# Performance work log

Measured on AMD Instinct MI355X. Metric: run time of the kernel, lower is better.

## Reference

```python
import jax, jax.numpy as jnp
import numpy as np

PS = 2      # patch_size
TOPK = 3    # topk


def setup_inputs() -> dict:
    key = jax.random.key(0)
    x = jax.random.normal(key, (8, 128, 64, 64), dtype=jnp.float32)
    alpha = jnp.asarray(5.0, dtype=jnp.float32)  # nn.Parameter alpha
    return {"x": x, "alpha": alpha}


def _forward(x, alpha):
    ps = PS
    b, c, h, w = x.shape
    nph, npw = h // ps, w // ps
    npatch = nph * npw
    pa = ps * ps
    # F.normalize(p=2, dim=-3) with torch eps=1e-12
    norm = jnp.maximum(jnp.sqrt(jnp.sum(x * x, axis=1, keepdims=True)), 1e-12)
    x = x / norm
    # patchify -> [b, c, npatch, patch_area] (patches h-major, pixels row-major)
    xp = x.reshape(b, c, nph, ps, npw, ps).transpose(0, 1, 2, 4, 3, 5)
    xp = xp.reshape(b, c, npatch, pa)
    diag_idx = jnp.arange(ps) * (ps + 1)  # [0, 3] for ps=2
    # gather diagonal pixels of each patch -> [b, ps, npatch, c]
    xd = xp[:, :, :, diag_idx].transpose(0, 3, 2, 1)
    # patch correlation matmul -> [b, ps, npatch, npatch]
    corr = jnp.einsum('bpnc,bpmc->bpnm', xd, xd)
    avg = jnp.mean(corr, axis=1, keepdims=True)
    s = jnp.concatenate([corr, avg], axis=1)  # [b, ps+1, npatch, npatch]
    # ZeroWindow gaussian mask (rat_s=0.05); channel index = patch center (r,c)
    sr, sc = 0.05 * nph, 0.05 * npw
    rr = jnp.arange(nph, dtype=jnp.float32)
    cc = jnp.arange(npw, dtype=jnp.float32)
    cent_r, cent_c = jnp.meshgrid(rr, cc, indexing='ij')
    cent_r = cent_r.reshape(npatch)
    cent_c = cent_c.reshape(npatch)
    gr = jnp.exp(-(rr[None, :] - cent_r[:, None]) ** 2 / (2.0 * sr * sr))  # [npatch, nph]
    gc = jnp.exp(-(cc[None, :] - cent_c[:, None]) ** 2 / (2.0 * sc * sc))  # [npatch, npw]
    mask = (1.0 - gr[:, :, None] * gc[:, None, :]).reshape(npatch, npatch)
    s = s * mask[None, None]
    a = s * alpha
    # double (row + col) softmax
    s = jax.nn.softmax(a, axis=-1) * jax.nn.softmax(a, axis=-2)
    # expand avg channel to all patch pixels, scatter diagonal channels back
    new_x = jnp.broadcast_to(s[:, -1:], (b, pa, npatch, npatch))
    new_x = new_x.at[:, diag_idx].set(s[:, :ps])
    # un-patchify second npatch axis to spatial [b, npatch, h, w]
    y = jnp.swapaxes(new_x, 1, 3)  # [b, npatch, npatch, pa]
    y = y.reshape(b, npatch, nph, npw, ps, ps).transpose(0, 1, 2, 4, 3, 5)
    y = y.reshape(b, npatch, h, w)
    # topk over the npatch axis (dim=-3)
    vals = jax.lax.top_k(jnp.moveaxis(y, 1, -1), TOPK)[0]  # [b, h, w, k]
    return jnp.moveaxis(vals, -1, 1)  # [b, k, h, w]


def reference(x, alpha):
    return _forward(x, alpha)
```

## Files before the change

### kernel.cpp

```cpp
#include <hip/hip_runtime.h>
#include <hip/hip_bf16.h>
#include <math.h>

#define NB 8
#define NC 128
#define NH 64
#define NW 64
#define NP 1024
#define TWO_SIG2 5.12f
#define LOG2E 1.44269504089f

static const size_t PSUM_OFF_B = 0;
static const size_t PBUF_OFF_B = (size_t)NB * 3 * 4 * NP * 4;
static const size_t XD_OFF_B   = PBUF_OFF_B + (size_t)NB * NP * 3 * 4 * 3 * 4;

typedef __bf16 bf16x8 __attribute__((ext_vector_type(8)));
typedef float f32x4 __attribute__((ext_vector_type(4)));

#define INSERT3(v, A, Bq, Cq)                          \
  {                                                    \
    const float _na = fmaxf(A, (v));                   \
    const float _nb = __builtin_amdgcn_fmed3f(A, Bq, (v)); \
    Cq = __builtin_amdgcn_fmed3f(Bq, Cq, (v));         \
    A = _na;                                           \
    Bq = _nb;                                          \
  }

#define MERGE3(a0, a1, a2, b0, b1, b2)       \
  {                                          \
    const float _x1 = fmaxf(a0, b0);         \
    const float _y1 = fminf(a0, b0);         \
    const float _x2 = fmaxf(a1, b1);         \
    const float _z  = fmaxf(a2, b2);         \
    a0 = _x1;                                \
    a1 = fmaxf(_y1, _x2);                    \
    a2 = fmaxf(fminf(_y1, _x2), _z);         \
  }

__global__ __launch_bounds__(1024) void k1_norm(const float* __restrict__ x,
                                                __hip_bfloat16* __restrict__ xd) {
  __shared__ __align__(16) float tile[NC * 65];
  const int chunk = blockIdx.x;
  const int p = blockIdx.y;
  const int b = blockIdx.z;
  const int t = threadIdx.x;
  const int pix = t & 63;
  const int cw = t >> 6;
  const int nbase = chunk * 64;

  {
    const int n = nbase + pix;
    const int i = ((n >> 5) << 1) + p;
    const int jf = (n & 31);
    const float* xb = x + (size_t)b * NC * NH * NW + (size_t)i * NW;
    for (int cc = 0; cc < 8; ++cc) {
      const int c = (cc << 4) + cw;
      const float2 v2 = ((const float2*)(xb + (size_t)c * NH * NW))[jf];
      tile[c * 65 + pix] = (p == 0) ? v2.x : v2.y;
    }
  }
  __syncthreads();

  const int lane = t & 63;
  const int w = t >> 6;
  for (int pg = 0; pg < 4; ++pg) {
    const int pixel = (pg << 4) + w;
    const float v0 = tile[lane * 65 + pixel];
    const float v1 = tile[(lane + 64) * 65 + pixel];
    float ss = v0 * v0 + v1 * v1;
#pragma unroll
    for (int m = 32; m >= 1; m >>= 1) ss += __shfl_xor(ss, m, 64);
    const float inv = 1.0f / fmaxf(sqrtf(ss), 1e-12f);
    __hip_bfloat16* xr = xd + ((size_t)((b * 2 + p) * NP) + nbase + pixel) * NC;
    xr[lane] = __float2bfloat16(v0 * inv);
    xr[lane + 64] = __float2bfloat16(v1 * inv);
  }
}

__global__ __launch_bounds__(256) void k2_sums(const ushort* __restrict__ xd,
                                               const float* __restrict__ alpha_p,
                                               float* __restrict__ psum) {
  __shared__ __align__(16) __bf16 Bs[2][64 * 136];
  const int t = threadIdx.x;
  const float K = (*alpha_p) * LOG2E;
  const float Cm = -(LOG2E / TWO_SIG2);

  const int cchunk = blockIdx.x;
  const int rowtile = blockIdx.y;
  const int b = blockIdx.z;
  const int i0 = rowtile << 6;
  const int jb = cchunk << 8;

  const int wave = t >> 6;
  const int lane = t & 63;
  const int lrow = lane & 15;
  const int kq = lane >> 4;

  const __bf16* X = (const __bf16*)xd;
  const __bf16* xp0 = X + ((size_t)(b * 2 + 0) * NP) * NC;
  const __bf16* xp1 = X + ((size_t)(b * 2 + 1) * NP) * NC;

  bf16x8 a0[4], a1[4];
  {
    const __bf16* pa0 = xp0 + (size_t)(i0 + wave * 16 + lrow) * NC + kq * 8;
    const __bf16* pa1 = xp1 + (size_t)(i0 + wave * 16 + lrow) * NC + kq * 8;
#pragma unroll
    for (int kc = 0; kc < 4; ++kc) {
      a0[kc] = *(const bf16x8*)(pa0 + kc * 32);
      a1[kc] = *(const bf16x8*)(pa1 + kc * 32);
    }
  }

  const int n0 = i0 + wave * 16 + kq * 4;
  const float rnf = (float)(n0 >> 5);
  const float cn0 = (float)(n0 & 31);

  float sums[3][4];
#pragma unroll
  for (int ch = 0; ch < 3; ++ch)
#pragma unroll
    for (int reg = 0; reg < 4; ++reg) sums[ch][reg] = 0.f;

  for (int sc = 0; sc < 4; ++sc) {
    const int j0 = jb + (sc << 6);
    if (sc) __syncthreads();
#pragma unroll
    for (int pl = 0; pl < 2; ++pl) {
      const float4* gb = (const float4*)(xd + ((size_t)(b * 2 + pl) * NP + j0) * NC);
#pragma unroll
      for (int it = 0; it < 4; ++it) {
        const int f = (it << 8) + t;
        const int r = f >> 4, q = f & 15;
        *(float4*)(&Bs[pl][r * 136 + q * 8]) = gb[f];
      }
    }
    __syncthreads();

    f32x4 acc[2][4];
#pragma unroll
    for (int pl = 0; pl < 2; ++pl)
#pragma unroll
      for (int ct = 0; ct < 4; ++ct)
#pragma unroll
        for (int u = 0; u < 4; ++u) acc[pl][ct][u] = 0.f;

#pragma unroll
    for (int kc = 0; kc < 4; ++kc) {
      const int kk = kc * 32 + (kq << 3);
#pragma unroll
      for (int ct = 0; ct < 4; ++ct) {
        const bf16x8 b0 = *(const bf16x8*)(&Bs[0][(ct * 16 + lrow) * 136 + kk]);
        const bf16x8 b1 = *(const bf16x8*)(&Bs[1][(ct * 16 + lrow) * 136 + kk]);
        acc[0][ct] = __builtin_amdgcn_mfma_f32_16x16x32_bf16(a0[kc], b0, acc[0][ct], 0, 0, 0);
        acc[1][ct] = __builtin_amdgcn_mfma_f32_16x16x32_bf16(a1[kc], b1, acc[1][ct], 0, 0, 0);
      }
    }

#pragma unroll
    for (int ct = 0; ct < 4; ++ct) {
      const int m = j0 + ct * 16 + lrow;
      const float rmf = (float)(m >> 5);
      const float cmf = (float)(m & 31);
      const float dr = rnf - rmf;
      const float dr2 = dr * dr;
#pragma unroll
      for (int reg = 0; reg < 4; ++reg) {
        const float dc = cn0 + (float)reg - cmf;
        const float d2 = fmaf(dc, dc, dr2);
        const float em = __builtin_amdgcn_exp2f(d2 * Cm);
        const float fm2 = fmaf(-em, K, K);
        const float g0 = fm2 * acc[0][ct][reg];
        const float g1 = fm2 * acc[1][ct][reg];
        sums[0][reg] += __builtin_amdgcn_exp2f(g0);
        sums[1][reg] += __builtin_amdgcn_exp2f(g1);
        sums[2][reg] += __builtin_amdgcn_exp2f(0.5f * (g0 + g1));
      }
    }
  }

#pragma unroll
  for (int off = 1; off < 16; off <<= 1)
#pragma unroll
    for (int ch = 0; ch < 3; ++ch)
#pragma unroll
      for (int reg = 0; reg < 4; ++reg)
        sums[ch][reg] += __shfl_xor(sums[ch][reg], off, 64);

  if (lrow == 0) {
#pragma unroll
    for (int ch = 0; ch < 3; ++ch)
#pragma unroll
      for (int reg = 0; reg < 4; ++reg) {
        const int n = i0 + wave * 16 + kq * 4 + reg;
        psum[(((size_t)b * 3 + ch) * 4 + cchunk) * NP + n] = sums[ch][reg];
      }
  }
}

__global__ __launch_bounds__(256) void k4_topk(const ushort* __restrict__ xd,
                                               const float* __restrict__ alpha_p,
                                               const float* __restrict__ psum,
                                               float* __restrict__ pbuf) {
  __shared__ __align__(16) __bf16 Bs[2][64 * 136];
  __shared__ float rsr[3][64];
  __shared__ float nlc[3][256];
  const int t = threadIdx.x;
  const float K = (*alpha_p) * LOG2E;
  const float Cm = -(LOG2E / TWO_SIG2);

  const int cchunk = blockIdx.x;
  const int rowtile = blockIdx.y;
  const int b = blockIdx.z;
  const int i0 = rowtile << 6;
  const int jb = cchunk << 8;

  if (t < 192) {
    const int ch = t >> 6, r = t & 63;
    const float* pp = psum + ((size_t)b * 3 + ch) * 4 * NP + i0 + r;
    rsr[ch][r] = 1.0f / (pp[0] + pp[NP] + pp[2 * NP] + pp[3 * NP]);
  }
#pragma unroll
  for (int ch = 0; ch < 3; ++ch) {
    const float* pp = psum + ((size_t)b * 3 + ch) * 4 * NP + jb + t;
    nlc[ch][t] = -__builtin_amdgcn_logf(pp[0] + pp[NP] + pp[2 * NP] + pp[3 * NP]);
  }

  const int wave = t >> 6;
  const int lane = t & 63;
  const int lrow = lane & 15;
  const int kq = lane >> 4;

  const __bf16* X = (const __bf16*)xd;
  const __bf16* xp0 = X + ((size_t)(b * 2 + 0) * NP) * NC;
  const __bf16* xp1 = X + ((size_t)(b * 2 + 1) * NP) * NC;

  bf16x8 a0[4], a1[4];
  {
    const __bf16* pa0 = xp0 + (size_t)(i0 + wave * 16 + lrow) * NC + kq * 8;
    const __bf16* pa1 = xp1 + (size_t)(i0 + wave * 16 + lrow) * NC + kq * 8;
#pragma unroll
    for (int kc = 0; kc < 4; ++kc) {
      a0[kc] = *(const bf16x8*)(pa0 + kc * 32);
      a1[kc] = *(const bf16x8*)(pa1 + kc * 32);
    }
  }

  const int n0 = i0 + wave * 16 + kq * 4;
  const float rnf = (float)(n0 >> 5);
  const float cn0 = (float)(n0 & 31);

  float tA[3][4], tB[3][4], tC[3][4];
#pragma unroll
  for (int ch = 0; ch < 3; ++ch)
#pragma unroll
    for (int reg = 0; reg < 4; ++reg) {
      tA[ch][reg] = -3.0e38f; tB[ch][reg] = -3.0e38f; tC[ch][reg] = -3.0e38f;
    }

  for (int sc = 0; sc < 4; ++sc) {
    const int j0 = jb + (sc << 6);
    __syncthreads();
#pragma unroll
    for (int pl = 0; pl < 2; ++pl) {
      const float4* gb = (const float4*)(xd + ((size_t)(b * 2 + pl) * NP + j0) * NC);
#pragma unroll
      for (int it = 0; it < 4; ++it) {
        const int f = (it << 8) + t;
        const int r = f >> 4, q = f & 15;
        *(float4*)(&Bs[pl][r * 136 + q * 8]) = gb[f];
      }
    }
    __syncthreads();

    f32x4 acc[2][4];
#pragma unroll
    for (int pl = 0; pl < 2; ++pl)
#pragma unroll
      for (int ct = 0; ct < 4; ++ct)
#pragma unroll
        for (int u = 0; u < 4; ++u) acc[pl][ct][u] = 0.f;

#pragma unroll
    for (int kc = 0; kc < 4; ++kc) {
      const int kk = kc * 32 + (kq << 3);
#pragma unroll
      for (int ct = 0; ct < 4; ++ct) {
        const bf16x8 b0 = *(const bf16x8*)(&Bs[0][(ct * 16 + lrow) * 136 + kk]);
        const bf16x8 b1 = *(const bf16x8*)(&Bs[1][(ct * 16 + lrow) * 136 + kk]);
        acc[0][ct] = __builtin_amdgcn_mfma_f32_16x16x32_bf16(a0[kc], b0, acc[0][ct], 0, 0, 0);
        acc[1][ct] = __builtin_amdgcn_mfma_f32_16x16x32_bf16(a1[kc], b1, acc[1][ct], 0, 0, 0);
      }
    }

#pragma unroll
    for (int ct = 0; ct < 4; ++ct) {
      const int mc = (sc << 6) + ct * 16 + lrow;
      const int m = jb + mc;
      const float rmf = (float)(m >> 5);
      const float cmf = (float)(m & 31);
      const float dr = rnf - rmf;
      const float dr2 = dr * dr;
      const float nl0 = nlc[0][mc];
      const float nl1 = nlc[1][mc];
      const float nl2 = nlc[2][mc];
#pragma unroll
      for (int reg = 0; reg < 4; ++reg) {
        const float dc = cn0 + (float)reg - cmf;
        const float d2 = fmaf(dc, dc, dr2);
        const float em = __builtin_amdgcn_exp2f(d2 * Cm);
        const float fm2 = fmaf(-em, K, K);
        const float f2 = fm2 + fm2;
        const float a0v = acc[0][ct][reg];
        const float a1v = acc[1][ct][reg];
        const float t0 = fmaf(f2, a0v, nl0);
        const float t1 = fmaf(f2, a1v, nl1);
        const float t2 = fmaf(fm2, a0v + a1v, nl2);
        INSERT3(t0, tA[0][reg], tB[0][reg], tC[0][reg]);
        INSERT3(t1, tA[1][reg], tB[1][reg], tC[1][reg]);
        INSERT3(t2, tA[2][reg], tB[2][reg], tC[2][reg]);
      }
    }
  }

#pragma unroll
  for (int off = 1; off < 16; off <<= 1)
#pragma unroll
    for (int ch = 0; ch < 3; ++ch)
#pragma unroll
      for (int reg = 0; reg < 4; ++reg) {
        const float b0 = __shfl_xor(tA[ch][reg], off, 64);
        const float b1 = __shfl_xor(tB[ch][reg], off, 64);
        const float b2 = __shfl_xor(tC[ch][reg], off, 64);
        MERGE3(tA[ch][reg], tB[ch][reg], tC[ch][reg], b0, b1, b2);
      }

  if (lrow == 0) {
#pragma unroll
    for (int ch = 0; ch < 3; ++ch)
#pragma unroll
      for (int reg = 0; reg < 4; ++reg) {
        const int nr = wave * 16 + kq * 4 + reg;
        const int n = i0 + nr;
        const float irn = rsr[ch][nr];
        const size_t base = ((((size_t)b * NP + n) * 3 + ch) * 4 + cchunk) * 3;
        pbuf[base + 0] = __builtin_amdgcn_exp2f(tA[ch][reg]) * irn;
        pbuf[base + 1] = __builtin_amdgcn_exp2f(tB[ch][reg]) * irn;
        pbuf[base + 2] = __builtin_amdgcn_exp2f(tC[ch][reg]) * irn;
      }
  }
}

__global__ __launch_bounds__(256) void k5_merge(const float* __restrict__ pbuf,
                                                float* __restrict__ out) {
  const int tau = blockIdx.x * 256 + threadIdx.x;
  const int b = tau >> 10;
  const int n = tau & (NP - 1);
  const int rn = n >> 5, cn = n & 31;

  float f0[3], f1[3], f2[3];
#pragma unroll
  for (int ch = 0; ch < 3; ++ch) {
    const size_t base = (((size_t)tau * 3 + ch) * 4) * 3;
    f0[ch] = pbuf[base + 0];
    f1[ch] = pbuf[base + 1];
    f2[ch] = pbuf[base + 2];
#pragma unroll
    for (int p = 1; p < 4; ++p) {
      const float b0 = pbuf[base + p * 3 + 0];
      const float b1 = pbuf[base + p * 3 + 1];
      const float b2 = pbuf[base + p * 3 + 2];
      MERGE3(f0[ch], f1[ch], f2[ch], b0, b1, b2);
    }
  }

  float* ob = out + (size_t)b * 3 * (NH * NW);
  const int i00 = ((rn << 1) * NW) + (cn << 1);
#pragma unroll
  for (int tt = 0; tt < 3; ++tt) {
    float* op = ob + (size_t)tt * (NH * NW);
    const float r0 = (tt == 0) ? f0[0] : (tt == 1) ? f1[0] : f2[0];
    const float r1 = (tt == 0) ? f0[1] : (tt == 1) ? f1[1] : f2[1];
    const float r2 = (tt == 0) ? f0[2] : (tt == 1) ? f1[2] : f2[2];
    op[i00] = r0;
    op[i00 + NW + 1] = r1;
    op[i00 + 1] = r2;
    op[i00 + NW] = r2;
  }
}

extern "C" void kernel_launch(void* const* d_in, const int* in_sizes, int n_in,
                              void* d_out, int out_size, void* d_ws, size_t ws_size,
                              hipStream_t stream) {
  const float* x = (const float*)d_in[0];
  const float* alpha = (const float*)d_in[1];
  float* out = (float*)d_out;
  char* ws = (char*)d_ws;

  float* psum = (float*)(ws + PSUM_OFF_B);
  float* pbuf = (float*)(ws + PBUF_OFF_B);
  __hip_bfloat16* xd = (__hip_bfloat16*)(ws + XD_OFF_B);

  k1_norm<<<dim3(16, 2, NB), 1024, 0, stream>>>(x, xd);
  k2_sums<<<dim3(4, 16, NB), 256, 0, stream>>>((const ushort*)xd, alpha, psum);
  k4_topk<<<dim3(4, 16, NB), 256, 0, stream>>>((const ushort*)xd, alpha, psum, pbuf);
  k5_merge<<<dim3(32), 256, 0, stream>>>(pbuf, out);
}
```

Measured before the change: 103.2 us.

## Fuse top-k candidate selection into sums pass, drop second matmul kernel

```diff
diff --git a/kernel.cpp b/kernel.cpp
--- a/kernel.cpp
+++ b/kernel.cpp
@@ -9,10 +9,11 @@
 #define NP 1024
 #define TWO_SIG2 5.12f
 #define LOG2E 1.44269504089f
+#define NT 6
 
 static const size_t PSUM_OFF_B = 0;
-static const size_t PBUF_OFF_B = (size_t)NB * 3 * 4 * NP * 4;
-static const size_t XD_OFF_B   = PBUF_OFF_B + (size_t)NB * NP * 3 * 4 * 3 * 4;
+static const size_t CAND_OFF_B = (size_t)NB * 3 * 4 * NP * 4;
+static const size_t XD_OFF_B   = CAND_OFF_B + (size_t)NB * NP * 3 * 4 * NT * 4;
 
 typedef __bf16 bf16x8 __attribute__((ext_vector_type(8)));
 typedef float f32x4 __attribute__((ext_vector_type(4)));
@@ -26,16 +27,18 @@
     Bq = _nb;                                          \
   }
 
-#define MERGE3(a0, a1, a2, b0, b1, b2)       \
-  {                                          \
-    const float _x1 = fmaxf(a0, b0);         \
-    const float _y1 = fminf(a0, b0);         \
-    const float _x2 = fmaxf(a1, b1);         \
-    const float _z  = fmaxf(a2, b2);         \
-    a0 = _x1;                                \
-    a1 = fmaxf(_y1, _x2);                    \
-    a2 = fmaxf(fminf(_y1, _x2), _z);         \
-  }
+#define INSERT4(v, A, Bq, Cq, Dq)                      \
+  {                                                    \
+    const float _na = fmaxf(A, (v));                   \
+    const float _nb = __builtin_amdgcn_fmed3f(A, Bq, (v)); \
+    const float _nc = __builtin_amdgcn_fmed3f(Bq, Cq, (v)); \
+    Dq = __builtin_amdgcn_fmed3f(Cq, Dq, (v));         \
+    A = _na; Bq = _nb; Cq = _nc;                       \
+  }
+
+__device__ __forceinline__ float packf(float g, unsigned idx) {
+  return __uint_as_float((__float_as_uint(g) & 0xFFFFFF00u) | idx);
+}
 
 __global__ __launch_bounds__(1024) void k1_norm(const float* __restrict__ x,
                                                 __hip_bfloat16* __restrict__ xd) {
@@ -79,8 +82,10 @@
 
 __global__ __launch_bounds__(256) void k2_sums(const ushort* __restrict__ xd,
                                                const float* __restrict__ alpha_p,
-                                               float* __restrict__ psum) {
+                                               float* __restrict__ psum,
+                                               float* __restrict__ cand) {
   __shared__ __align__(16) __bf16 Bs[2][64 * 136];
+  __shared__ float stage[64][3][NT];
   const int t = threadIdx.x;
   const float K = (*alpha_p) * LOG2E;
   const float Cm = -(LOG2E / TWO_SIG2);
@@ -116,10 +121,15 @@
   const float cn0 = (float)(n0 & 31);
 
   float sums[3][4];
+  float Lc[3][4][4];
 #pragma unroll
   for (int ch = 0; ch < 3; ++ch)
 #pragma unroll
-    for (int reg = 0; reg < 4; ++reg) sums[ch][reg] = 0.f;
+    for (int reg = 0; reg < 4; ++reg) {
+      sums[ch][reg] = 0.f;
+#pragma unroll
+      for (int q = 0; q < 4; ++q) Lc[ch][reg][q] = -3.0e38f;
+    }
 
   for (int sc = 0; sc < 4; ++sc) {
     const int j0 = jb + (sc << 6);
@@ -158,11 +168,13 @@
 
 #pragma unroll
     for (int ct = 0; ct < 4; ++ct) {
-      const int m = j0 + ct * 16 + lrow;
+      const int mc = (sc << 6) + ct * 16 + lrow;
+      const int m = jb + mc;
       const float rmf = (float)(m >> 5);
       const float cmf = (float)(m & 31);
       const float dr = rnf - rmf;
       const float dr2 = dr * dr;
+      const unsigned mcu = (unsigned)mc;
 #pragma unroll
       for (int reg = 0; reg < 4; ++reg) {
         const float dc = cn0 + (float)reg - cmf;
@@ -174,6 +186,12 @@
         sums[0][reg] += __builtin_amdgcn_exp2f(g0);
         sums[1][reg] += __builtin_amdgcn_exp2f(g1);
         sums[2][reg] += __builtin_amdgcn_exp2f(0.5f * (g0 + g1));
+        const float p0 = packf(g0, mcu);
+        const float p1 = packf(g1, mcu);
+        const float p2 = packf(g0 + g1, mcu);
+        INSERT4(p0, Lc[0][reg][0], Lc[0][reg][1], Lc[0][reg][2], Lc[0][reg][3]);
+        INSERT4(p1, Lc[1][reg][0], Lc[1][reg][1], Lc[1][reg][2], Lc[1][reg][3]);
+        INSERT4(p2, Lc[2][reg][0], Lc[2][reg][1], Lc[2][reg][2], Lc[2][reg][3]);
       }
     }
   }
@@ -195,192 +213,96 @@
         psum[(((size_t)b * 3 + ch) * 4 + cchunk) * NP + n] = sums[ch][reg];
       }
   }
-}
-
-__global__ __launch_bounds__(256) void k4_topk(const ushort* __restrict__ xd,
-                                               const float* __restrict__ alpha_p,
-                                               const float* __restrict__ psum,
-                                               float* __restrict__ pbuf) {
-  __shared__ __align__(16) __bf16 Bs[2][64 * 136];
-  __shared__ float rsr[3][64];
-  __shared__ float nlc[3][256];
+
+#pragma unroll
+  for (int ch = 0; ch < 3; ++ch)
+#pragma unroll
+    for (int reg = 0; reg < 4; ++reg) {
+      float l0 = Lc[ch][reg][0], l1 = Lc[ch][reg][1];
+      float l2 = Lc[ch][reg][2], l3 = Lc[ch][reg][3];
+      const int np = wave * 16 + kq * 4 + reg;
+#pragma unroll
+      for (int r = 0; r < NT; ++r) {
+        float mx = l0;
+        mx = fmaxf(mx, __shfl_xor(mx, 1, 64));
+        mx = fmaxf(mx, __shfl_xor(mx, 2, 64));
+        mx = fmaxf(mx, __shfl_xor(mx, 4, 64));
+        mx = fmaxf(mx, __shfl_xor(mx, 8, 64));
+        if (lrow == 0) stage[np][ch][r] = mx;
+        const bool own = (l0 == mx);
+        l0 = own ? l1 : l0;
+        l1 = own ? l2 : l1;
+        l2 = own ? l3 : l2;
+        l3 = own ? -3.0e38f : l3;
+      }
+    }
+  __syncthreads();
+
+  for (int u = t; u < 64 * 3 * NT; u += 256) {
+    const int np = u / (3 * NT);
+    const int rem = u - np * (3 * NT);
+    const int ch = rem / NT;
+    const int r = rem - ch * NT;
+    cand[(((size_t)b * NP + i0 + np) * 3 + ch) * (4 * NT) + cchunk * NT + r] =
+        stage[np][ch][r];
+  }
+}
+
+__global__ __launch_bounds__(256) void k5_final(const float* __restrict__ cand,
+                                                const float* __restrict__ psum,
+                                                float* __restrict__ out) {
+  __shared__ float nlR[3][NP];
   const int t = threadIdx.x;
-  const float K = (*alpha_p) * LOG2E;
-  const float Cm = -(LOG2E / TWO_SIG2);
-
-  const int cchunk = blockIdx.x;
-  const int rowtile = blockIdx.y;
-  const int b = blockIdx.z;
-  const int i0 = rowtile << 6;
-  const int jb = cchunk << 8;
-
-  if (t < 192) {
-    const int ch = t >> 6, r = t & 63;
-    const float* pp = psum + ((size_t)b * 3 + ch) * 4 * NP + i0 + r;
-    rsr[ch][r] = 1.0f / (pp[0] + pp[NP] + pp[2 * NP] + pp[3 * NP]);
-  }
-#pragma unroll
-  for (int ch = 0; ch < 3; ++ch) {
-    const float* pp = psum + ((size_t)b * 3 + ch) * 4 * NP + jb + t;
-    nlc[ch][t] = -__builtin_amdgcn_logf(pp[0] + pp[NP] + pp[2 * NP] + pp[3 * NP]);
-  }
-
-  const int wave = t >> 6;
-  const int lane = t & 63;
-  const int lrow = lane & 15;
-  const int kq = lane >> 4;
-
-  const __bf16* X = (const __bf16*)xd;
-  const __bf16* xp0 = X + ((size_t)(b * 2 + 0) * NP) * NC;
-  const __bf16* xp1 = X + ((size_t)(b * 2 + 1) * NP) * NC;
-
-  bf16x8 a0[4], a1[4];
-  {
-    const __bf16* pa0 = xp0 + (size_t)(i0 + wave * 16 + lrow) * NC + kq * 8;
-    const __bf16* pa1 = xp1 + (size_t)(i0 + wave * 16 + lrow) * NC + kq * 8;
-#pragma unroll
-    for (int kc = 0; kc < 4; ++kc) {
-      a0[kc] = *(const bf16x8*)(pa0 + kc * 32);
-      a1[kc] = *(const bf16x8*)(pa1 + kc * 32);
-    }
-  }
-
-  const int n0 = i0 + wave * 16 + kq * 4;
-  const float rnf = (float)(n0 >> 5);
-  const float cn0 = (float)(n0 & 31);
-
-  float tA[3][4], tB[3][4], tC[3][4];
-#pragma unroll
-  for (int ch = 0; ch < 3; ++ch)
-#pragma unroll
-    for (int reg = 0; reg < 4; ++reg) {
-      tA[ch][reg] = -3.0e38f; tB[ch][reg] = -3.0e38f; tC[ch][reg] = -3.0e38f;
-    }
-
-  for (int sc = 0; sc < 4; ++sc) {
-    const int j0 = jb + (sc << 6);
-    __syncthreads();
-#pragma unroll
-    for (int pl = 0; pl < 2; ++pl) {
-      const float4* gb = (const float4*)(xd + ((size_t)(b * 2 + pl) * NP + j0) * NC);
-#pragma unroll
-      for (int it = 0; it < 4; ++it) {
-        const int f = (it << 8) + t;
-        const int r = f >> 4, q = f & 15;
-        *(float4*)(&Bs[pl][r * 136 + q * 8]) = gb[f];
-      }
-    }
-    __syncthreads();
-
-    f32x4 acc[2][4];
-#pragma unroll
-    for (int pl = 0; pl < 2; ++pl)
-#pragma unroll
-      for (int ct = 0; ct < 4; ++ct)
-#pragma unroll
-        for (int u = 0; u < 4; ++u) acc[pl][ct][u] = 0.f;
-
-#pragma unroll
-    for (int kc = 0; kc < 4; ++kc) {
-      const int kk = kc * 32 + (kq << 3);
-#pragma unroll
-      for (int ct = 0; ct < 4; ++ct) {
-        const bf16x8 b0 = *(const bf16x8*)(&Bs[0][(ct * 16 + lrow) * 136 + kk]);
-        const bf16x8 b1 = *(const bf16x8*)(&Bs[1][(ct * 16 + lrow) * 136 + kk]);
-        acc[0][ct] = __builtin_amdgcn_mfma_f32_16x16x32_bf16(a0[kc], b0, acc[0][ct], 0, 0, 0);
-        acc[1][ct] = __builtin_amdgcn_mfma_f32_16x16x32_bf16(a1[kc], b1, acc[1][ct], 0, 0, 0);
-      }
-    }
-
-#pragma unroll
-    for (int ct = 0; ct < 4; ++ct) {
-      const int mc = (sc << 6) + ct * 16 + lrow;
-      const int m = jb + mc;
-      const float rmf = (float)(m >> 5);
-      const float cmf = (float)(m & 31);
-      const float dr = rnf - rmf;
-      const float dr2 = dr * dr;
-      const float nl0 = nlc[0][mc];
-      const float nl1 = nlc[1][mc];
-      const float nl2 = nlc[2][mc];
-#pragma unroll
-      for (int reg = 0; reg < 4; ++reg) {
-        const float dc = cn0 + (float)reg - cmf;
-        const float d2 = fmaf(dc, dc, dr2);
-        const float em = __builtin_amdgcn_exp2f(d2 * Cm);
-        const float fm2 = fmaf(-em, K, K);
-        const float f2 = fm2 + fm2;
-        const float a0v = acc[0][ct][reg];
-        const float a1v = acc[1][ct][reg];
-        const float t0 = fmaf(f2, a0v, nl0);
-        const float t1 = fmaf(f2, a1v, nl1);
-        const float t2 = fmaf(fm2, a0v + a1v, nl2);
-        INSERT3(t0, tA[0][reg], tB[0][reg], tC[0][reg]);
-        INSERT3(t1, tA[1][reg], tB[1][reg], tC[1][reg]);
-        INSERT3(t2, tA[2][reg], tB[2][reg], tC[2][reg]);
-      }
-    }
-  }
-
-#pragma unroll
-  for (int off = 1; off < 16; off <<= 1)
-#pragma unroll
-    for (int ch = 0; ch < 3; ++ch)
-#pragma unroll
-      for (int reg = 0; reg < 4; ++reg) {
-        const float b0 = __shfl_xor(tA[ch][reg], off, 64);
-        const float b1 = __shfl_xor(tB[ch][reg], off, 64);
-        const float b2 = __shfl_xor(tC[ch][reg], off, 64);
-        MERGE3(tA[ch][reg], tB[ch][reg], tC[ch][reg], b0, b1, b2);
-      }
-
-  if (lrow == 0) {
-#pragma unroll
-    for (int ch = 0; ch < 3; ++ch)
-#pragma unroll
-      for (int reg = 0; reg < 4; ++reg) {
-        const int nr = wave * 16 + kq * 4 + reg;
-        const int n = i0 + nr;
-        const float irn = rsr[ch][nr];
-        const size_t base = ((((size_t)b * NP + n) * 3 + ch) * 4 + cchunk) * 3;
-        pbuf[base + 0] = __builtin_amdgcn_exp2f(tA[ch][reg]) * irn;
-        pbuf[base + 1] = __builtin_amdgcn_exp2f(tB[ch][reg]) * irn;
-        pbuf[base + 2] = __builtin_amdgcn_exp2f(tC[ch][reg]) * irn;
-      }
-  }
-}
-
-__global__ __launch_bounds__(256) void k5_merge(const float* __restrict__ pbuf,
-                                                float* __restrict__ out) {
-  const int tau = blockIdx.x * 256 + threadIdx.x;
+  const int tau = blockIdx.x * 256 + t;
   const int b = tau >> 10;
   const int n = tau & (NP - 1);
+
+#pragma unroll
+  for (int ch = 0; ch < 3; ++ch)
+#pragma unroll
+    for (int k = 0; k < 4; ++k) {
+      const int m = (k << 8) + t;
+      const float* pp = psum + ((size_t)b * 3 + ch) * 4 * NP + m;
+      nlR[ch][m] = -__builtin_amdgcn_logf(pp[0] + pp[NP] + pp[2 * NP] + pp[3 * NP]);
+    }
+  __syncthreads();
+
+  float irn[3];
+#pragma unroll
+  for (int ch = 0; ch < 3; ++ch) {
+    const float* pp = psum + ((size_t)b * 3 + ch) * 4 * NP + n;
+    irn[ch] = 1.0f / (pp[0] + pp[NP] + pp[2 * NP] + pp[3 * NP]);
+  }
+
+  float o0[3], o1[3], o2[3];
+#pragma unroll
+  for (int ch = 0; ch < 3; ++ch) {
+    float tA = -3.0e38f, tB = -3.0e38f, tC = -3.0e38f;
+    const float cf = (ch == 2) ? 1.0f : 2.0f;
+    const float* cp = cand + (((size_t)b * NP + n) * 3 + ch) * (4 * NT);
+#pragma unroll
+    for (int cc = 0; cc < 4; ++cc)
+#pragma unroll
+      for (int r = 0; r < NT; ++r) {
+        const float p = cp[cc * NT + r];
+        const int mi = (cc << 8) | (int)(__float_as_uint(p) & 255u);
+        const float tv = fmaf(cf, p, nlR[ch][mi]);
+        INSERT3(tv, tA, tB, tC);
+      }
+    o0[ch] = __builtin_amdgcn_exp2f(tA) * irn[ch];
+    o1[ch] = __builtin_amdgcn_exp2f(tB) * irn[ch];
+    o2[ch] = __builtin_amdgcn_exp2f(tC) * irn[ch];
+  }
+
   const int rn = n >> 5, cn = n & 31;
-
-  float f0[3], f1[3], f2[3];
-#pragma unroll
-  for (int ch = 0; ch < 3; ++ch) {
-    const size_t base = (((size_t)tau * 3 + ch) * 4) * 3;
-    f0[ch] = pbuf[base + 0];
-    f1[ch] = pbuf[base + 1];
-    f2[ch] = pbuf[base + 2];
-#pragma unroll
-    for (int p = 1; p < 4; ++p) {
-      const float b0 = pbuf[base + p * 3 + 0];
-      const float b1 = pbuf[base + p * 3 + 1];
-      const float b2 = pbuf[base + p * 3 + 2];
-      MERGE3(f0[ch], f1[ch], f2[ch], b0, b1, b2);
-    }
-  }
-
   float* ob = out + (size_t)b * 3 * (NH * NW);
   const int i00 = ((rn << 1) * NW) + (cn << 1);
 #pragma unroll
   for (int tt = 0; tt < 3; ++tt) {
     float* op = ob + (size_t)tt * (NH * NW);
-    const float r0 = (tt == 0) ? f0[0] : (tt == 1) ? f1[0] : f2[0];
-    const float r1 = (tt == 0) ? f0[1] : (tt == 1) ? f1[1] : f2[1];
-    const float r2 = (tt == 0) ? f0[2] : (tt == 1) ? f1[2] : f2[2];
+    const float r0 = (tt == 0) ? o0[0] : (tt == 1) ? o1[0] : o2[0];
+    const float r1 = (tt == 0) ? o0[1] : (tt == 1) ? o1[1] : o2[1];
+    const float r2 = (tt == 0) ? o0[2] : (tt == 1) ? o1[2] : o2[2];
     op[i00] = r0;
     op[i00 + NW + 1] = r1;
     op[i00 + 1] = r2;
@@ -397,11 +319,10 @@
   char* ws = (char*)d_ws;
 
   float* psum = (float*)(ws + PSUM_OFF_B);
-  float* pbuf = (float*)(ws + PBUF_OFF_B);
+  float* cand = (float*)(ws + CAND_OFF_B);
   __hip_bfloat16* xd = (__hip_bfloat16*)(ws + XD_OFF_B);
 
   k1_norm<<<dim3(16, 2, NB), 1024, 0, stream>>>(x, xd);
-  k2_sums<<<dim3(4, 16, NB), 256, 0, stream>>>((const ushort*)xd, alpha, psum);
-  k4_topk<<<dim3(4, 16, NB), 256, 0, stream>>>((const ushort*)xd, alpha, psum, pbuf);
-  k5_merge<<<dim3(32), 256, 0, stream>>>(pbuf, out);
-}
+  k2_sums<<<dim3(4, 16, NB), 256, 0, stream>>>((const ushort*)xd, alpha, psum, cand);
+  k5_final<<<dim3(32), 256, 0, stream>>>(cand, psum, out);
+}
```

After: 103.3 us. No clear change (+0.1%).
